# Optimization experiments

Measured on AMD Instinct MI355X. Metric: run time of the kernel, lower is better.

## Reference

```python
import jax, jax.numpy as jnp
import numpy as np

# Structure constants (equal-sized graphs; first SPG nodes of each graph are sentence nodes)
B = 64          # graphs in batch
NPG = 1024      # nodes per graph
SPG = 64        # sentence nodes per graph
N = B * NPG     # 65536 total nodes
E = 524288      # total edges (within-graph)
C = 256         # in_channels
H = 512         # TopKPooling hardcoded hidden
KS = 3          # num_output_sentences
KO = int(np.ceil(0.5 * (NPG - SPG)))  # ratio=0.5 -> 480 'other' nodes kept per graph
SLOPE = 0.01    # LeakyReLU default negative slope


def gcn_conv(x, row, col, w, W, b, n):
    """PyG GCNConv with edge_weight: add self-loops (weight 1), symmetric norm, aggregate at col."""
    loop = jnp.arange(n, dtype=row.dtype)
    row2 = jnp.concatenate([row, loop])
    col2 = jnp.concatenate([col, loop])
    w2 = jnp.concatenate([w, jnp.ones((n,), w.dtype)])
    deg = jax.ops.segment_sum(w2, col2, num_segments=n)
    dinv = jnp.where(deg > 0, jax.lax.rsqrt(jnp.where(deg > 0, deg, 1.0)), 0.0)
    norm = dinv[row2] * w2 * dinv[col2]          # [E+N]
    h = x @ W                                     # [N, out]
    out = jax.ops.segment_sum(norm[:, None] * h[row2], col2, num_segments=n)
    return out + b


def setup_inputs() -> dict:
    key = jax.random.key(0)
    ks = jax.random.split(key, 6)
    x = jax.random.normal(ks[0], (N, C), jnp.float32)
    # within-graph random edges
    gid = jnp.arange(E, dtype=jnp.int32) // (E // B)
    src = jax.random.randint(ks[1], (E,), 0, NPG, dtype=jnp.int32) + gid * NPG
    dst = jax.random.randint(ks[2], (E,), 0, NPG, dtype=jnp.int32) + gid * NPG
    edge_index = jnp.stack([src, dst], axis=0)
    edge_attr = jax.random.uniform(ks[3], (E, 1), jnp.float32, 0.1, 1.0)
    batch = jnp.repeat(jnp.arange(B, dtype=jnp.int32), NPG)
    W1 = jax.random.normal(ks[4], (C, H), jnp.float32) * (1.0 / np.sqrt(C))
    b1 = jnp.zeros((H,), jnp.float32)
    W2 = jax.random.normal(ks[5], (H, 1), jnp.float32) * (1.0 / np.sqrt(H))
    b2 = jnp.zeros((1,), jnp.float32)
    return {"x": x, "edge_index": edge_index, "edge_attr": edge_attr, "batch": batch,
            "W1": W1, "b1": b1, "W2": W2, "b2": b2}


def reference(x, edge_index, edge_attr, batch, W1, b1, W2, b2):
    row, col = edge_index[0], edge_index[1]
    w = edge_attr[:, 0]                           # edge_weight = edge_attr.squeeze()
    # 2-layer GCN scorer
    h = gcn_conv(x, row, col, w, W1, b1, N)
    h = jnp.where(h > 0, h, SLOPE * h)            # LeakyReLU
    score = gcn_conv(h, row, col, w, W2, b2, N)[:, 0]
    score = jnp.nan_to_num(score)
    sg = score.reshape(B, NPG)                    # dense per-graph scores (graphs equal-sized)
    # per-graph top-k: 3 sentence nodes, ceil(0.5*other) other nodes
    _, si = jax.lax.top_k(sg[:, :SPG], KS)        # [B, KS] local idx among sentence nodes
    sent_perm = (si + jnp.arange(B)[:, None] * NPG).reshape(-1)
    _, oi = jax.lax.top_k(sg[:, SPG:], KO)        # [B, KO] local idx among other nodes
    other_perm = (oi + SPG + jnp.arange(B)[:, None] * NPG).reshape(-1)
    perm = jnp.concatenate([sent_perm, other_perm])  # [B*(KS+KO)]
    # gather + scale (multiplier = 1)
    score_perm = score[perm]
    x_out = x[perm] * score_perm[:, None]
    batch_out = batch[perm]
    # filter_adj (padded: dropped edges marked -1 / zeroed; 'keep' mask returned)
    mask = jnp.full((N,), -1, dtype=perm.dtype).at[perm].set(jnp.arange(perm.shape[0], dtype=perm.dtype))
    nr, nc = mask[row], mask[col]
    keep = (nr >= 0) & (nc >= 0)
    ei_new = jnp.where(keep, jnp.stack([nr, nc], axis=0), -1)
    ea_new = jnp.where(keep[:, None], edge_attr, 0.0)
    sentence_scores = sg[:, :SPG].reshape(-1)
    sentence_batch = jnp.repeat(jnp.arange(B, dtype=batch.dtype), SPG)
    return (x_out, ei_new, ea_new, batch_out, perm, score_perm, sentence_scores, sentence_batch, keep)
```

## Files before the change

kernel.cpp:

```cpp
#include <hip/hip_runtime.h>

#define NN   65536
#define NE   524288
#define EPG  8192

#define O1 7913472
#define O2 8962048
#define O3 9486336
#define O4 9517248
#define O5 9548160
#define O6 9579072
#define O7 9583168
#define O8 9587264

#define CSR_OFF    8388608
#define DINV_OFF   9437184
#define Z_OFF      9502720
#define W1HI_OFF   9568256
#define RSTART_OFF 9633792
#define CURSOR_OFF 9699344
#define W1LO_OFF   9764880
#define HIST_OFF   9830416
#define SCORE_OFF  65536
#define YLO_OFF    4194304

typedef __attribute__((ext_vector_type(8))) short bfrag;
typedef __attribute__((ext_vector_type(4))) float f32x4;
typedef __attribute__((ext_vector_type(8))) unsigned short us8;
typedef __attribute__((ext_vector_type(2))) unsigned long long u64x2;

__device__ __forceinline__ unsigned monof(float f) {
  unsigned u = __float_as_uint(f);
  return (u & 0x80000000u) ? ~u : (u | 0x80000000u);
}

__device__ __forceinline__ unsigned short bf16rne(float f) {
  unsigned u = __float_as_uint(f);
  return (unsigned short)((u + 0x7FFFu + ((u >> 16) & 1u)) >> 16);
}

__global__ __launch_bounds__(256) void k_zero_w1t(unsigned long long* __restrict__ hist,
    float* __restrict__ z, const float* __restrict__ W1,
    unsigned short* __restrict__ hi, unsigned short* __restrict__ lo) {
  __shared__ unsigned short sh[64][72], sl[64][72];
  int b = blockIdx.x, t = threadIdx.x;
  if (b < 256) {
    int n = b * 256 + t;
    hist[n] = 0ull;
    z[n] = 0.0f;
    return;
  }
  int bb = b - 256;
  int bk = bb & 3, bc = bb >> 2;
  int k0 = bk * 64, c0 = bc * 64;
#pragma unroll
  for (int s = 0; s < 16; ++s) {
    int i = t + s * 256;
    int k = i >> 6, c = i & 63;
    float v = W1[(k0 + k) * 512 + c0 + c];
    unsigned short h = bf16rne(v);
    float hf = __uint_as_float((unsigned)h << 16);
    sh[c][k] = h;
    sl[c][k] = bf16rne(v - hf);
  }
  __syncthreads();
#pragma unroll
  for (int s = 0; s < 16; ++s) {
    int i = t + s * 256;
    int c = i >> 6, k = i & 63;
    hi[(c0 + c) * 256 + k0 + k] = sh[c][k];
    lo[(c0 + c) * 256 + k0 + k] = sl[c][k];
  }
}

__global__ void k_hist(const int* __restrict__ ei, const float* __restrict__ w,
                       unsigned long long* __restrict__ hist) {
  int e = blockIdx.x * 256 + threadIdx.x;
  if (e < NE) {
    int c = ei[NE + e];
    unsigned long long add = (1ull << 40) |
        (unsigned long long)(unsigned)__float2uint_rn(w[e] * 1048576.0f);
    atomicAdd(&hist[c], add);
  }
}

__global__ __launch_bounds__(256) void k_prefix(const unsigned long long* __restrict__ hist,
    unsigned* __restrict__ rstart, unsigned* __restrict__ cursor, float* __restrict__ dinv) {
  __shared__ unsigned tmp[2][256];
  int g = blockIdx.x, t = threadIdx.x;
  int base = g << 10;
  unsigned c[4], sum = 0;
  unsigned long long hv[4];
#pragma unroll
  for (int u = 0; u < 4; ++u) {
    hv[u] = hist[base + t * 4 + u];
    c[u] = (unsigned)(hv[u] >> 40);
    sum += c[u];
  }
  tmp[0][t] = sum;
  __syncthreads();
  int pin = 0;
  for (int off = 1; off < 256; off <<= 1) {
    int pout = pin ^ 1;
    unsigned v = tmp[pin][t];
    if (t >= off) v += tmp[pin][t - off];
    tmp[pout][t] = v;
    __syncthreads();
    pin = pout;
  }
  unsigned run = (t == 0) ? 0u : tmp[pin][t - 1];
#pragma unroll
  for (int u = 0; u < 4; ++u) {
    unsigned pos = (unsigned)(g << 13) + run;
    rstart[base + t * 4 + u] = pos;
    cursor[base + t * 4 + u] = pos;
    run += c[u];
  }
#pragma unroll
  for (int u = 0; u < 4; ++u) {
    int n = base + t * 4 + u;
    float wsum = 1.0f + (float)(hv[u] & ((1ull << 40) - 1)) * 9.5367431640625e-07f;
    dinv[n] = rsqrtf(wsum);
  }
  if (g == 0 && t == 0) rstart[NN] = NE;
}

__global__ void k_scatter(const int* __restrict__ ei, const float* __restrict__ w,
                          const float* __restrict__ dinv, unsigned* __restrict__ cursor,
                          unsigned long long* __restrict__ csr) {
  int e = blockIdx.x * 256 + threadIdx.x;
  if (e < NE) {
    int r = ei[e], c = ei[NE + e];
    float cf = w[e] * dinv[r] * dinv[c];
    unsigned pos = atomicAdd(&cursor[c], 1u);
    unsigned sl = (unsigned)(r & 1023);
    csr[pos] = ((unsigned long long)__float_as_uint(cf) << 32) |
               (sl << 15) | (sl * 18u);
  }
}

__global__ __launch_bounds__(1024, 1) void k_aggx(const float* __restrict__ x,
    const unsigned long long* __restrict__ csr, const unsigned* __restrict__ rstart,
    const float* __restrict__ dinv, unsigned short* __restrict__ yhi,
    unsigned short* __restrict__ ylo, int gbase) {
  __shared__ float xs[1024 * 18];
  __shared__ unsigned long long es[8193];
  __shared__ unsigned rp[1025];
  __shared__ float dv2[1024];
  int bid = blockIdx.x;
  int g  = bid & 31;
  int cc = bid >> 5;
  int gg = gbase + g;
  int c0 = cc * 16;
  int t = threadIdx.x;
  int nbase = gg << 10;
  unsigned ebase = (unsigned)gg << 13;
  {
    rp[t] = rstart[nbase + t] - ebase;
    float dv = dinv[nbase + t];
    dv2[t] = dv * dv;
  }
  if (t == 0) { rp[1024] = 8192u; es[8192] = 0ull; }
  {
    const u64x2* src = (const u64x2*)(csr + ebase);
    u64x2* dst = (u64x2*)es;
#pragma unroll
    for (int i = 0; i < 4; ++i)
      dst[t + i * 1024] = src[t + i * 1024];
  }
#pragma unroll
  for (int s = 0; s < 4; ++s) {
    int i = t + s * 1024;
    int row = i >> 2, q = (i & 3) * 4;
    float4 v = *(const float4*)&x[(nbase + row) * 256 + c0 + q];
    float* d = &xs[row * 18 + q];
    *(float2*)&d[0] = make_float2(v.x, v.y);
    *(float2*)&d[2] = make_float2(v.z, v.w);
  }
  __syncthreads();
  int jj = t & 7;
  int h  = (t >> 3) & 1;
  int grp = t >> 4;
  int dbase = grp * 16;
  int j2 = 2 * jj;
  for (int dd = 0; dd < 8; ++dd) {
    int d0 = dbase + dd;
    unsigned pA = rp[d0], qA = rp[d0 + 1];
    unsigned pB = rp[d0 + 8], qB = rp[d0 + 9];
    int L0 = (int)(qA - pA), L1 = (int)(qB - pB);
    int L = L0 > L1 ? L0 : L1;
    int d = d0 + 8 * h;
    unsigned p = h ? pB : pA;
    unsigned q = h ? qB : qA;
    float2 xv = *(const float2*)&xs[d * 18 + j2];
    float dv = dv2[d];
    float ax = dv * xv.x, ay = dv * xv.y;
    for (int k = 0; k < L; k += 4) {
      unsigned long long cv[4];
#pragma unroll
      for (int u = 0; u < 4; ++u) {
        unsigned a = p + (unsigned)(k + u);
        cv[u] = es[a < q ? a : 8192u];
      }
#pragma unroll
      for (int u = 0; u < 4; ++u) {
        float cf = __uint_as_float((unsigned)(cv[u] >> 32));
        const float2 xr = *(const float2*)&xs[((unsigned)cv[u] & 0x7FFFu) + j2];
        ax += cf * xr.x;
        ay += cf * xr.y;
      }
    }
    int idx = ((g << 10) + d) * 256 + c0 + j2;
    unsigned short hx = bf16rne(ax), hy = bf16rne(ay);
    float lx = ax - __uint_as_float((unsigned)hx << 16);
    float ly = ay - __uint_as_float((unsigned)hy << 16);
    *(unsigned*)&yhi[idx] = (unsigned)hx | ((unsigned)hy << 16);
    *(unsigned*)&ylo[idx] = (unsigned)bf16rne(lx) | ((unsigned)bf16rne(ly) << 16);
  }
}

__global__ __launch_bounds__(256, 3) void k_gemm(
    const unsigned short* __restrict__ yhi, const unsigned short* __restrict__ ylo,
    const unsigned short* __restrict__ w1hi, const unsigned short* __restrict__ w1lo,
    const float* __restrict__ b1, const float* __restrict__ W2,
    float* __restrict__ z, int node_base) {
  __shared__ unsigned short Ah_s[128 * 40], Al_s[128 * 40];
  __shared__ unsigned short Bh_s[128 * 40], Bl_s[128 * 40];
  int bx = blockIdx.x & 3, by = blockIdx.x >> 2;
  int r0 = by * 128, c0 = bx * 128;
  int t = threadIdx.x;
  int lane = t & 63, wid = t >> 6;
  int wr = wid >> 1, wc = wid & 1;
  int lr = lane & 15, hg = lane >> 4;
  f32x4 acc[4][4];
#pragma unroll
  for (int m = 0; m < 4; ++m)
#pragma unroll
    for (int n = 0; n < 4; ++n)
      acc[m][n] = (f32x4){0.0f, 0.0f, 0.0f, 0.0f};
  int rr = t >> 2, kq = (t & 3) * 8;
  for (int kt = 0; kt < 256; kt += 32) {
    us8 va0 = *(const us8*)&yhi[(r0 + rr) * 256 + kt + kq];
    us8 va1 = *(const us8*)&yhi[(r0 + rr + 64) * 256 + kt + kq];
    us8 vb0 = *(const us8*)&ylo[(r0 + rr) * 256 + kt + kq];
    us8 vb1 = *(const us8*)&ylo[(r0 + rr + 64) * 256 + kt + kq];
    us8 vc0 = *(const us8*)&w1hi[(c0 + rr) * 256 + kt + kq];
    us8 vc1 = *(const us8*)&w1hi[(c0 + rr + 64) * 256 + kt + kq];
    us8 vd0 = *(const us8*)&w1lo[(c0 + rr) * 256 + kt + kq];
    us8 vd1 = *(const us8*)&w1lo[(c0 + rr + 64) * 256 + kt + kq];
    __syncthreads();
    *(us8*)&Ah_s[rr * 40 + kq] = va0;  *(us8*)&Ah_s[(rr + 64) * 40 + kq] = va1;
    *(us8*)&Al_s[rr * 40 + kq] = vb0;  *(us8*)&Al_s[(rr + 64) * 40 + kq] = vb1;
    *(us8*)&Bh_s[rr * 40 + kq] = vc0;  *(us8*)&Bh_s[(rr + 64) * 40 + kq] = vc1;
    *(us8*)&Bl_s[rr * 40 + kq] = vd0;  *(us8*)&Bl_s[(rr + 64) * 40 + kq] = vd1;
    __syncthreads();
    bfrag Ah[4], Al[4], Bh[4], Bl[4];
#pragma unroll
    for (int m = 0; m < 4; ++m) {
      int ra = (wr * 64 + m * 16 + lr) * 40 + hg * 8;
      Ah[m] = *(const bfrag*)&Ah_s[ra];
      Al[m] = *(const bfrag*)&Al_s[ra];
      int rb = (wc * 64 + m * 16 + lr) * 40 + hg * 8;
      Bh[m] = *(const bfrag*)&Bh_s[rb];
      Bl[m] = *(const bfrag*)&Bl_s[rb];
    }
#pragma unroll
    for (int m = 0; m < 4; ++m)
#pragma unroll
      for (int n = 0; n < 4; ++n) {
        acc[m][n] = __builtin_amdgcn_mfma_f32_16x16x32_bf16(Ah[m], Bh[n], acc[m][n], 0, 0, 0);
        acc[m][n] = __builtin_amdgcn_mfma_f32_16x16x32_bf16(Ah[m], Bl[n], acc[m][n], 0, 0, 0);
        acc[m][n] = __builtin_amdgcn_mfma_f32_16x16x32_bf16(Al[m], Bh[n], acc[m][n], 0, 0, 0);
      }
  }
  float p[4][4];
#pragma unroll
  for (int m = 0; m < 4; ++m)
#pragma unroll
    for (int i = 0; i < 4; ++i) p[m][i] = 0.0f;
#pragma unroll
  for (int n = 0; n < 4; ++n) {
    int col = c0 + wc * 64 + n * 16 + lr;
    float b1v = b1[col], w2v = W2[col];
#pragma unroll
    for (int m = 0; m < 4; ++m)
#pragma unroll
      for (int i = 0; i < 4; ++i) {
        float v = acc[m][n][i] + b1v;
        v = v > 0.0f ? v : 0.01f * v;
        p[m][i] += v * w2v;
      }
  }
#pragma unroll
  for (int off = 8; off > 0; off >>= 1)
#pragma unroll
    for (int m = 0; m < 4; ++m)
#pragma unroll
      for (int i = 0; i < 4; ++i)
        p[m][i] += __shfl_xor(p[m][i], off, 16);
  if (lr == 0) {
    int rbase = node_base + r0 + wr * 64 + hg * 4;
#pragma unroll
    for (int m = 0; m < 4; ++m)
#pragma unroll
      for (int i = 0; i < 4; ++i)
        unsafeAtomicAdd(&z[rbase + m * 16 + i], p[m][i]);
  }
}

__global__ void k_score(const unsigned long long* __restrict__ csr,
                        const unsigned* __restrict__ rstart,
                        const float* __restrict__ dinv, const float* __restrict__ z,
                        const float* __restrict__ b2, float* __restrict__ score,
                        int* __restrict__ mask) {
  int n = blockIdx.x * 256 + threadIdx.x;
  if (n >= NN) return;
  mask[n] = -1;
  int nb = n & ~1023;
  float dv = dinv[n];
  float a = b2[0] + dv * dv * z[n];
  unsigned s = rstart[n], epos = rstart[n + 1];
  for (unsigned e = s; e < epos; ++e) {
    unsigned long long p = csr[e];
    a += __uint_as_float((unsigned)(p >> 32)) * z[nb + (((unsigned)p >> 15) & 1023u)];
  }
  score[n] = a;
}

__device__ void bitonic(unsigned long long* keys, int n, int t, int nt) {
  for (int k = 2; k <= n; k <<= 1)
    for (int jj = k >> 1; jj > 0; jj >>= 1) {
      __syncthreads();
      for (int i = t; i < n; i += nt) {
        int ixj = i ^ jj;
        if (ixj > i) {
          unsigned long long a = keys[i], c = keys[ixj];
          bool up = ((i & k) == 0);
          if ((a > c) == up) { keys[i] = c; keys[ixj] = a; }
        }
      }
    }
  __syncthreads();
}

__global__ __launch_bounds__(512) void k_topk(const float* __restrict__ score,
                                              int* __restrict__ mask,
                                              float* __restrict__ out) {
  __shared__ unsigned long long keys[1024];
  int b = blockIdx.x, t = threadIdx.x;
  int base = b << 10;
  if (t < 64) {
    float v = score[base + t];
    keys[t] = ((unsigned long long)(~monof(v)) << 32) | (unsigned)t;
    out[O6 + b * 64 + t] = v;
    out[O7 + b * 64 + t] = (float)b;
  }
  __syncthreads();
  bitonic(keys, 64, t, 512);
  if (t < 3) {
    int idx = (int)(keys[t] & 0xFFFFFFFFull);
    int node = base + idx;
    int pos = b * 3 + t;
    mask[node] = pos;
    out[O4 + pos] = (float)node;
    out[O5 + pos] = score[node];
    out[O3 + pos] = (float)b;
  }
  __syncthreads();
  for (int i = t; i < 1024; i += 512) {
    if (i < 960) {
      float v = score[base + 64 + i];
      keys[i] = ((unsigned long long)(~monof(v)) << 32) | (unsigned)i;
    } else {
      keys[i] = 0xFFFFFFFFFFFFFFFFull;
    }
  }
  __syncthreads();
  bitonic(keys, 1024, t, 512);
  for (int r = t; r < 480; r += 512) {
    int idx = (int)(keys[r] & 0xFFFFFFFFull);
    int node = base + 64 + idx;
    int pos = 192 + b * 480 + r;
    mask[node] = pos;
    out[O4 + pos] = (float)node;
    out[O5 + pos] = score[node];
    out[O3 + pos] = (float)b;
  }
}

__global__ __launch_bounds__(256) void k_tail(const int* __restrict__ ei,
    const float* __restrict__ w, const int* __restrict__ mask,
    const float* __restrict__ x, float* __restrict__ out) {
  int bid = blockIdx.x, t = threadIdx.x;
  if (bid < 2048) {
    int e = bid * 256 + t;
    int nr = mask[ei[e]];
    int nc = mask[ei[NE + e]];
    bool keep = (nr >= 0) && (nc >= 0);
    out[O1 + e]      = keep ? (float)nr : -1.0f;
    out[O1 + NE + e] = keep ? (float)nc : -1.0f;
    out[O2 + e]      = keep ? w[e] : 0.0f;
    out[O8 + e]      = keep ? 1.0f : 0.0f;
  } else {
    int i = (bid - 2048) * 4 + (t >> 6);
    int lane = t & 63;
    int node = (int)out[O4 + i];
    float s = out[O5 + i];
    float4 v = ((const float4*)&x[node * 256])[lane];
    ((float4*)&out[i * 256])[lane] = make_float4(v.x * s, v.y * s, v.z * s, v.w * s);
  }
}

extern "C" void kernel_launch(void* const* d_in, const int* in_sizes, int n_in,
                              void* d_out, int out_size, void* d_ws, size_t ws_size,
                              hipStream_t stream) {
  (void)in_sizes; (void)n_in; (void)out_size; (void)d_ws; (void)ws_size;
  const float* x  = (const float*)d_in[0];
  const int*   ei = (const int*)d_in[1];
  const float* w  = (const float*)d_in[2];
  const float* W1 = (const float*)d_in[4];
  const float* b1 = (const float*)d_in[5];
  const float* W2 = (const float*)d_in[6];
  const float* b2 = (const float*)d_in[7];
  float* out    = (float*)d_out;
  unsigned short* yhi = (unsigned short*)out;
  unsigned short* ylo = (unsigned short*)(out + YLO_OFF);
  unsigned long long* csr = (unsigned long long*)(out + CSR_OFF);
  float* dinv   = out + DINV_OFF;
  float* z      = out + Z_OFF;
  unsigned* rstart = (unsigned*)(out + RSTART_OFF);
  unsigned* cursor = (unsigned*)(out + CURSOR_OFF);
  unsigned long long* hist64 = (unsigned long long*)(out + HIST_OFF);
  unsigned short* w1hi = (unsigned short*)(out + W1HI_OFF);
  unsigned short* w1lo = (unsigned short*)(out + W1LO_OFF);
  float* score  = out + SCORE_OFF;
  int*   mask   = (int*)d_out;

  k_zero_w1t<<<288, 256, 0, stream>>>(hist64, z, W1, w1hi, w1lo);
  k_hist<<<2048, 256, 0, stream>>>(ei, w, hist64);
  k_prefix<<<64, 256, 0, stream>>>(hist64, rstart, cursor, dinv);
  k_scatter<<<2048, 256, 0, stream>>>(ei, w, dinv, cursor, csr);
  for (int ch = 0; ch < 2; ++ch) {
    k_aggx<<<512, 1024, 0, stream>>>(x, csr, rstart, dinv, yhi, ylo, ch * 32);
    k_gemm<<<1024, 256, 0, stream>>>(yhi, ylo, w1hi, w1lo, b1, W2, z, ch * 32768);
  }
  k_score<<<256, 256, 0, stream>>>(csr, rstart, dinv, z, b2, score, mask);
  k_topk<<<64, 512, 0, stream>>>(score, mask, out);
  k_tail<<<2048 + 7728, 256, 0, stream>>>(ei, w, mask, x, out);
}
```

Before: 240.4 us.

## Fuse score computation into top-k kernel and shrink aggregation LDS row pitch

Merges the per-node score kernel into the per-graph top-k kernel, so scores stay in shared memory and are never written to or reread from global memory, and one launch goes away. The top-k block grows to 1024 threads, one node per thread. Separately, the aggregation kernel's shared x tile row stride drops from 18 to 17 floats, with scalar loads replacing float2, to change the LDS bank-conflict pattern and reduce LDS footprint. The fused score stage now runs on only 64 blocks instead of 256, which lowers parallelism for the CSR gather.

Measured after the change: 225.5 us. -6.2%, faster.

```diff
diff --git a/kernel.cpp b/kernel.cpp
--- a/kernel.cpp
+++ b/kernel.cpp
@@ -21,7 +21,6 @@
 #define CURSOR_OFF 9699344
 #define W1LO_OFF   9764880
 #define HIST_OFF   9830416
-#define SCORE_OFF  65536
 #define YLO_OFF    4194304
 
 typedef __attribute__((ext_vector_type(8))) short bfrag;
@@ -135,7 +134,7 @@
     unsigned pos = atomicAdd(&cursor[c], 1u);
     unsigned sl = (unsigned)(r & 1023);
     csr[pos] = ((unsigned long long)__float_as_uint(cf) << 32) |
-               (sl << 15) | (sl * 18u);
+               (sl << 15) | (sl * 17u);
   }
 }
 
@@ -143,7 +142,7 @@
     const unsigned long long* __restrict__ csr, const unsigned* __restrict__ rstart,
     const float* __restrict__ dinv, unsigned short* __restrict__ yhi,
     unsigned short* __restrict__ ylo, int gbase) {
-  __shared__ float xs[1024 * 18];
+  __shared__ float xs[1024 * 17];
   __shared__ unsigned long long es[8193];
   __shared__ unsigned rp[1025];
   __shared__ float dv2[1024];
@@ -173,9 +172,8 @@
     int i = t + s * 1024;
     int row = i >> 2, q = (i & 3) * 4;
     float4 v = *(const float4*)&x[(nbase + row) * 256 + c0 + q];
-    float* d = &xs[row * 18 + q];
-    *(float2*)&d[0] = make_float2(v.x, v.y);
-    *(float2*)&d[2] = make_float2(v.z, v.w);
+    float* d = &xs[row * 17 + q];
+    d[0] = v.x; d[1] = v.y; d[2] = v.z; d[3] = v.w;
   }
   __syncthreads();
   int jj = t & 7;
@@ -192,9 +190,9 @@
     int d = d0 + 8 * h;
     unsigned p = h ? pB : pA;
     unsigned q = h ? qB : qA;
-    float2 xv = *(const float2*)&xs[d * 18 + j2];
+    int dofs = d * 17 + j2;
     float dv = dv2[d];
-    float ax = dv * xv.x, ay = dv * xv.y;
+    float ax = dv * xs[dofs], ay = dv * xs[dofs + 1];
     for (int k = 0; k < L; k += 4) {
       unsigned long long cv[4];
 #pragma unroll
@@ -205,9 +203,9 @@
 #pragma unroll
       for (int u = 0; u < 4; ++u) {
         float cf = __uint_as_float((unsigned)(cv[u] >> 32));
-        const float2 xr = *(const float2*)&xs[((unsigned)cv[u] & 0x7FFFu) + j2];
-        ax += cf * xr.x;
-        ay += cf * xr.y;
+        unsigned o = ((unsigned)cv[u] & 0x7FFFu) + (unsigned)j2;
+        ax += cf * xs[o];
+        ay += cf * xs[o + 1];
       }
     }
     int idx = ((g << 10) + d) * 256 + c0 + j2;
@@ -308,25 +306,6 @@
   }
 }
 
-__global__ void k_score(const unsigned long long* __restrict__ csr,
-                        const unsigned* __restrict__ rstart,
-                        const float* __restrict__ dinv, const float* __restrict__ z,
-                        const float* __restrict__ b2, float* __restrict__ score,
-                        int* __restrict__ mask) {
-  int n = blockIdx.x * 256 + threadIdx.x;
-  if (n >= NN) return;
-  mask[n] = -1;
-  int nb = n & ~1023;
-  float dv = dinv[n];
-  float a = b2[0] + dv * dv * z[n];
-  unsigned s = rstart[n], epos = rstart[n + 1];
-  for (unsigned e = s; e < epos; ++e) {
-    unsigned long long p = csr[e];
-    a += __uint_as_float((unsigned)(p >> 32)) * z[nb + (((unsigned)p >> 15) & 1023u)];
-  }
-  score[n] = a;
-}
-
 __device__ void bitonic(unsigned long long* keys, int n, int t, int nt) {
   for (int k = 2; k <= n; k <<= 1)
     for (int jj = k >> 1; jj > 0; jj >>= 1) {
@@ -343,47 +322,53 @@
   __syncthreads();
 }
 
-__global__ __launch_bounds__(512) void k_topk(const float* __restrict__ score,
-                                              int* __restrict__ mask,
-                                              float* __restrict__ out) {
+__global__ __launch_bounds__(1024) void k_score_topk(
+    const unsigned long long* __restrict__ csr, const unsigned* __restrict__ rstart,
+    const float* __restrict__ dinv, const float* __restrict__ z,
+    const float* __restrict__ b2, int* __restrict__ mask, float* __restrict__ out) {
+  __shared__ float sc[1024];
   __shared__ unsigned long long keys[1024];
   int b = blockIdx.x, t = threadIdx.x;
   int base = b << 10;
+  int n = base + t;
+  mask[n] = -1;
+  float dv = dinv[n];
+  float a = b2[0] + dv * dv * z[n];
+  unsigned s = rstart[n], epos = rstart[n + 1];
+  for (unsigned e = s; e < epos; ++e) {
+    unsigned long long p = csr[e];
+    a += __uint_as_float((unsigned)(p >> 32)) * z[base + (((unsigned)p >> 15) & 1023u)];
+  }
+  sc[t] = a;
   if (t < 64) {
-    float v = score[base + t];
-    keys[t] = ((unsigned long long)(~monof(v)) << 32) | (unsigned)t;
-    out[O6 + b * 64 + t] = v;
+    out[O6 + b * 64 + t] = a;
     out[O7 + b * 64 + t] = (float)b;
-  }
-  __syncthreads();
-  bitonic(keys, 64, t, 512);
+    keys[t] = ((unsigned long long)(~monof(a)) << 32) | (unsigned)t;
+  }
+  __syncthreads();
+  bitonic(keys, 64, t, 1024);
   if (t < 3) {
     int idx = (int)(keys[t] & 0xFFFFFFFFull);
     int node = base + idx;
     int pos = b * 3 + t;
     mask[node] = pos;
     out[O4 + pos] = (float)node;
-    out[O5 + pos] = score[node];
+    out[O5 + pos] = sc[idx];
     out[O3 + pos] = (float)b;
   }
   __syncthreads();
-  for (int i = t; i < 1024; i += 512) {
-    if (i < 960) {
-      float v = score[base + 64 + i];
-      keys[i] = ((unsigned long long)(~monof(v)) << 32) | (unsigned)i;
-    } else {
-      keys[i] = 0xFFFFFFFFFFFFFFFFull;
-    }
-  }
-  __syncthreads();
-  bitonic(keys, 1024, t, 512);
-  for (int r = t; r < 480; r += 512) {
-    int idx = (int)(keys[r] & 0xFFFFFFFFull);
+  keys[t] = (t < 960)
+      ? (((unsigned long long)(~monof(sc[64 + t])) << 32) | (unsigned)t)
+      : 0xFFFFFFFFFFFFFFFFull;
+  __syncthreads();
+  bitonic(keys, 1024, t, 1024);
+  if (t < 480) {
+    int idx = (int)(keys[t] & 0xFFFFFFFFull);
     int node = base + 64 + idx;
-    int pos = 192 + b * 480 + r;
+    int pos = 192 + b * 480 + t;
     mask[node] = pos;
     out[O4 + pos] = (float)node;
-    out[O5 + pos] = score[node];
+    out[O5 + pos] = sc[64 + idx];
     out[O3 + pos] = (float)b;
   }
 }
@@ -433,7 +418,6 @@
   unsigned long long* hist64 = (unsigned long long*)(out + HIST_OFF);
   unsigned short* w1hi = (unsigned short*)(out + W1HI_OFF);
   unsigned short* w1lo = (unsigned short*)(out + W1LO_OFF);
-  float* score  = out + SCORE_OFF;
   int*   mask   = (int*)d_out;
 
   k_zero_w1t<<<288, 256, 0, stream>>>(hist64, z, W1, w1hi, w1lo);
@@ -444,7 +428,6 @@
     k_aggx<<<512, 1024, 0, stream>>>(x, csr, rstart, dinv, yhi, ylo, ch * 32);
     k_gemm<<<1024, 256, 0, stream>>>(yhi, ylo, w1hi, w1lo, b1, W2, z, ch * 32768);
   }
-  k_score<<<256, 256, 0, stream>>>(csr, rstart, dinv, z, b2, score, mask);
-  k_topk<<<64, 512, 0, stream>>>(score, mask, out);
+  k_score_topk<<<64, 1024, 0, stream>>>(csr, rstart, dinv, z, b2, mask, out);
   k_tail<<<2048 + 7728, 256, 0, stream>>>(ei, w, mask, x, out);
 }
```
